# Kernel tuning notes

Hardware: AMD Instinct MI355X
Metric: run time of the kernel (lower is better)

The kernel has to match this reference:

```python
import jax, jax.numpy as jnp
import numpy as np

EMB = 1024

def setup_inputs() -> dict:
    key = jax.random.key(0)
    ks = jax.random.split(key, 7)
    s = 1.0 / np.sqrt(EMB)
    x = jax.random.normal(ks[0], (4, 2048, EMB), dtype=jnp.float32)
    Wk = jax.random.normal(ks[1], (EMB, EMB), dtype=jnp.float32) * s
    bk = jnp.zeros((EMB,), dtype=jnp.float32)
    Wq = jax.random.normal(ks[2], (EMB, EMB), dtype=jnp.float32) * s
    bq = jnp.zeros((EMB,), dtype=jnp.float32)
    Wv = jax.random.normal(ks[3], (EMB, EMB), dtype=jnp.float32) * s
    bv = jnp.zeros((EMB,), dtype=jnp.float32)
    return {"x": x, "Wk": Wk, "bk": bk, "Wq": Wq, "bq": bq, "Wv": Wv, "bv": bv}

def reference(x, Wk, bk, Wq, bq, Wv, bv):
    # Linear layers: x @ W.T + b (torch nn.Linear convention)
    k = jnp.einsum('bse,fe->bsf', x, Wk) + bk
    q = jnp.einsum('bse,fe->bsf', x, Wq) + bq
    v = jnp.einsum('bse,fe->bsf', x, Wv) + bv
    E = x.shape[-1]
    # NOTE: original computes k @ q^T (not q @ k^T) — reproduce faithfully.
    sim = jnp.einsum('bsd,btd->bst', k, q) / jnp.sqrt(jnp.float32(E))
    S = x.shape[1]
    causal = jnp.tril(jnp.ones((S, S), dtype=bool))  # [S,S]
    sim = jnp.where(causal, sim, -jnp.inf)
    attn = jax.nn.softmax(sim, axis=-1)
    return jnp.einsum('bst,btd->bsd', attn, v)
```

## Files before the change

### kernel.cpp

```cpp
#include <hip/hip_runtime.h>
#include <cstdint>


typedef __attribute__((ext_vector_type(8))) _Float16 f16x8;
typedef __attribute__((ext_vector_type(4))) float f32x4;

__device__ __forceinline__ unsigned short f2h(float x) {
  return __builtin_bit_cast(unsigned short, (_Float16)x);
}

__device__ __forceinline__ void lds_dma16(const void* g, void* l) {
  auto gp = reinterpret_cast<const __attribute__((address_space(1))) void*>(
      reinterpret_cast<uintptr_t>(g));
  auto lp = reinterpret_cast<__attribute__((address_space(3))) void*>(
      reinterpret_cast<uintptr_t>(l));
  __builtin_amdgcn_global_load_lds(gp, lp, 16, 0, 0);
}

__device__ __forceinline__ void gemm128(const unsigned short* __restrict__ Ag,
                                        const unsigned short* __restrict__ Bg,
                                        int lda, int ldb, int nk,
                                        unsigned short* As, unsigned short* Bs,
                                        f32x4 acc[4][4]) {
  const int tid = threadIdx.x;
  const int lane = tid & 63, wave = tid >> 6;
  const int wm = wave >> 1, wn = wave & 1;
  const int sr = lane >> 2;
  const int scb = (((lane & 3) ^ ((lane >> 3) & 3)) * 8);
  const int rr = lane & 15, qq = lane >> 4;
  const int slot = ((qq ^ ((rr >> 1) & 3)) * 8);

#pragma unroll
  for (int i = 0; i < 4; ++i)
#pragma unroll
    for (int j = 0; j < 4; ++j) {
      f32x4 z = {0.f, 0.f, 0.f, 0.f};
      acc[i][j] = z;
    }

  for (int k0 = 0; k0 < nk; k0 += 32) {
#pragma unroll
    for (int c = 0; c < 2; ++c) {
      int chunk = wave * 2 + c;
      int row = chunk * 16 + sr;
      lds_dma16(Ag + (size_t)row * lda + k0 + scb, As + chunk * 512);
      lds_dma16(Bg + (size_t)row * ldb + k0 + scb, Bs + chunk * 512);
    }
    __syncthreads();

    f16x8 af[4], bf[4];
    const unsigned short* Ar = As + (wm * 64 + rr) * 32 + slot;
    const unsigned short* Br = Bs + (wn * 64 + rr) * 32 + slot;
#pragma unroll
    for (int i = 0; i < 4; ++i) af[i] = *(const f16x8*)(Ar + i * 512);
#pragma unroll
    for (int j = 0; j < 4; ++j) bf[j] = *(const f16x8*)(Br + j * 512);
#pragma unroll
    for (int i = 0; i < 4; ++i)
#pragma unroll
      for (int j = 0; j < 4; ++j)
        acc[i][j] = __builtin_amdgcn_mfma_f32_16x16x32_f16(af[i], bf[j],
                                                           acc[i][j], 0, 0, 0);
    __syncthreads();
  }
}

__global__ void cvt_kernel(const float* __restrict__ x,
                           const float* __restrict__ w0,
                           const float* __restrict__ w1,
                           const float* __restrict__ w2,
                           unsigned short* __restrict__ dst) {
  int i = blockIdx.x * 256 + threadIdx.x;
  const float* s;
  size_t si;
  if (i < 2097152) {
    s = x; si = i;
  } else {
    int j = i - 2097152;
    int z = j >> 18;
    s = (z == 0) ? w0 : ((z == 1) ? w1 : w2);
    si = j & 262143;
  }
  float4 f = ((const float4*)s)[si];
  ushort4 u;
  u.x = f2h(f.x); u.y = f2h(f.y); u.z = f2h(f.z); u.w = f2h(f.w);
  ((ushort4*)dst)[i] = u;
}

__global__ __launch_bounds__(256) void qkv_gemm_kernel(
    const unsigned short* __restrict__ xh, const unsigned short* __restrict__ wh,
    const float* __restrict__ bk, const float* __restrict__ bq,
    const float* __restrict__ bv, unsigned short* __restrict__ kh,
    unsigned short* __restrict__ qh, unsigned short* __restrict__ vh) {
  __shared__ unsigned short As[128 * 32], Bs[128 * 32];
  const int tn = blockIdx.x & 7, z = blockIdx.x >> 3;
  const unsigned short* W = wh + (size_t)z * 1048576;
  const float* bias = (z == 0) ? bk : ((z == 1) ? bq : bv);
  unsigned short* dst = (z == 0) ? kh : ((z == 1) ? qh : vh);
  const int tm = blockIdx.y;

  f32x4 acc[4][4];
  gemm128(xh + (size_t)tm * 128 * 1024, W + (size_t)tn * 128 * 1024,
          1024, 1024, 1024, As, Bs, acc);

  const int lane = threadIdx.x & 63, wave = threadIdx.x >> 6;
  const int wm = wave >> 1, wn = wave & 1, rr = lane & 15, qq = lane >> 4;
  float bj[4];
#pragma unroll
  for (int j = 0; j < 4; ++j)
    bj[j] = bias[tn * 128 + wn * 64 + j * 16 + rr];
#pragma unroll
  for (int i = 0; i < 4; ++i)
#pragma unroll
    for (int reg = 0; reg < 4; ++reg) {
      int gm = tm * 128 + wm * 64 + i * 16 + qq * 4 + reg;
#pragma unroll
      for (int j = 0; j < 4; ++j) {
        int gc = tn * 128 + wn * 64 + j * 16 + rr;
        dst[(size_t)gm * 1024 + gc] = f2h(acc[i][j][reg] + bj[j]);
      }
    }
}

__global__ void transpose_v_kernel(const unsigned short* __restrict__ v,
                                   unsigned short* __restrict__ vT) {
  __shared__ unsigned short tile[32][33];
  const int b = blockIdx.z;
  const unsigned short* vp = v + (size_t)b * 2048 * 1024;
  unsigned short* vtp = vT + (size_t)b * 1024 * 2048;
  const int t0 = blockIdx.x * 32, d0 = blockIdx.y * 32;
  const int x = threadIdx.x, y = threadIdx.y;
#pragma unroll
  for (int i = 0; i < 32; i += 8)
    tile[y + i][x] = vp[(size_t)(t0 + y + i) * 1024 + d0 + x];
  __syncthreads();
#pragma unroll
  for (int i = 0; i < 32; i += 8)
    vtp[(size_t)(d0 + y + i) * 2048 + t0 + x] = tile[x][y + i];
}

__global__ __launch_bounds__(256) void scores_kernel(
    const unsigned short* __restrict__ kh, const unsigned short* __restrict__ qh,
    unsigned short* __restrict__ P, float* __restrict__ rsum) {
  const int tt = blockIdx.x, ts = blockIdx.y, b = blockIdx.z;
  if (tt > ts) return;
  __shared__ unsigned short As[128 * 32], Bs[128 * 32];

  f32x4 acc[4][4];
  gemm128(kh + ((size_t)(b * 2048 + ts * 128)) * 1024,
          qh + ((size_t)(b * 2048 + tt * 128)) * 1024,
          1024, 1024, 1024, As, Bs, acc);

  const int lane = threadIdx.x & 63, wave = threadIdx.x >> 6;
  const int wm = wave >> 1, wn = wave & 1, rr = lane & 15, qq = lane >> 4;
  unsigned short* Pb = P + (size_t)b * 2048 * 2048;
  float* rs = rsum + b * 2048;
#pragma unroll
  for (int i = 0; i < 4; ++i)
#pragma unroll
    for (int reg = 0; reg < 4; ++reg) {
      int srow = ts * 128 + wm * 64 + i * 16 + qq * 4 + reg;
      float p = 0.f;
#pragma unroll
      for (int j = 0; j < 4; ++j) {
        int tcol = tt * 128 + wn * 64 + j * 16 + rr;
        float e = (tcol <= srow) ? __expf(acc[i][j][reg] * 0.03125f - 4.0f)
                                 : 0.0f;
        Pb[(size_t)srow * 2048 + tcol] = f2h(e);
        p += e;
      }
#pragma unroll
      for (int off = 1; off < 16; off <<= 1) p += __shfl_xor(p, off);
      if (rr == 0) atomicAdd(rs + srow, p);
    }
}

__global__ __launch_bounds__(256) void pv_gemm_kernel(
    const unsigned short* __restrict__ P, const unsigned short* __restrict__ vT,
    const float* __restrict__ rsum, float* __restrict__ out) {
  const int td = blockIdx.x, ts = 15 - blockIdx.y, b = blockIdx.z;
  __shared__ unsigned short As[128 * 32], Bs[128 * 32];

  f32x4 acc[4][4];
  gemm128(P + ((size_t)(b * 2048 + ts * 128)) * 2048,
          vT + ((size_t)(b * 1024 + td * 128)) * 2048,
          2048, 2048, (ts + 1) * 128, As, Bs, acc);

  const int lane = threadIdx.x & 63, wave = threadIdx.x >> 6;
  const int wm = wave >> 1, wn = wave & 1, rr = lane & 15, qq = lane >> 4;
#pragma unroll
  for (int i = 0; i < 4; ++i)
#pragma unroll
    for (int reg = 0; reg < 4; ++reg) {
      int srow = ts * 128 + wm * 64 + i * 16 + qq * 4 + reg;
      float rv = __builtin_amdgcn_rcpf(rsum[b * 2048 + srow]);
#pragma unroll
      for (int j = 0; j < 4; ++j) {
        int dcol = td * 128 + wn * 64 + j * 16 + rr;
        out[((size_t)(b * 2048 + srow)) * 1024 + dcol] = acc[i][j][reg] * rv;
      }
    }
}

extern "C" void kernel_launch(void* const* d_in, const int* in_sizes, int n_in,
                              void* d_out, int out_size, void* d_ws,
                              size_t ws_size, hipStream_t stream) {
  const float* x  = (const float*)d_in[0];
  const float* Wk = (const float*)d_in[1];
  const float* bk = (const float*)d_in[2];
  const float* Wq = (const float*)d_in[3];
  const float* bq = (const float*)d_in[4];
  const float* Wv = (const float*)d_in[5];
  const float* bv = (const float*)d_in[6];
  float* out = (float*)d_out;

  char* ws = (char*)d_ws;
  const size_t MB = 1ull << 20;
  unsigned short* xh = (unsigned short*)(ws + 0);
  unsigned short* wh = (unsigned short*)(ws + 16 * MB);
  unsigned short* vh = (unsigned short*)(ws + 22 * MB);
  unsigned short* P  = (unsigned short*)(ws + 0);
  unsigned short* kh = (unsigned short*)(ws + 38 * MB);
  unsigned short* qh = (unsigned short*)(ws + 54 * MB);
  unsigned short* vT = (unsigned short*)(ws + 70 * MB);
  float* rsum = (float*)(ws + 86 * MB);

  hipMemsetAsync(rsum, 0, 8192 * sizeof(float), stream);
  cvt_kernel<<<11264, 256, 0, stream>>>(x, Wk, Wq, Wv, xh);
  qkv_gemm_kernel<<<dim3(24, 64), 256, 0, stream>>>(xh, wh, bk, bq, bv,
                                                    kh, qh, vh);
  transpose_v_kernel<<<dim3(64, 32, 4), dim3(32, 8), 0, stream>>>(vh, vT);
  scores_kernel<<<dim3(16, 16, 4), 256, 0, stream>>>(kh, qh, P, rsum);
  pv_gemm_kernel<<<dim3(8, 16, 4), 256, 0, stream>>>(P, vT, rsum, out);
}
```

Baseline: 277.2 us.

## Double GEMM K-step to 64, fold rsum clear, vectorize transpose, compact causal grid

The shared GEMM loop now stages 64-wide K slices per barrier pair, with a new XOR swizzle, which halves the number of syncthreads and gives each wave more MFMA work per load. The rsum memset is folded into the conversion kernel as extra threads. The V transpose uses 64x64 tiles with ushort4 global accesses. The scores launch maps a linear index onto lower-triangle tiles only, so no blocks exit early. Doubling the LDS tile per block may reduce occupancy.

```diff
diff --git a/kernel.cpp b/kernel.cpp
--- a/kernel.cpp
+++ b/kernel.cpp
@@ -25,10 +25,11 @@
   const int tid = threadIdx.x;
   const int lane = tid & 63, wave = tid >> 6;
   const int wm = wave >> 1, wn = wave & 1;
-  const int sr = lane >> 2;
-  const int scb = (((lane & 3) ^ ((lane >> 3) & 3)) * 8);
+  const int sr = lane >> 3;
+  const int scb = ((lane & 7) ^ sr) * 8;
   const int rr = lane & 15, qq = lane >> 4;
-  const int slot = ((qq ^ ((rr >> 1) & 3)) * 8);
+  const int slot0 = ((qq) ^ (rr & 7)) * 8;
+  const int slot1 = ((4 + qq) ^ (rr & 7)) * 8;
 
 #pragma unroll
   for (int i = 0; i < 4; ++i)
@@ -38,29 +39,44 @@
       acc[i][j] = z;
     }
 
-  for (int k0 = 0; k0 < nk; k0 += 32) {
-#pragma unroll
-    for (int c = 0; c < 2; ++c) {
-      int chunk = wave * 2 + c;
-      int row = chunk * 16 + sr;
+  for (int k0 = 0; k0 < nk; k0 += 64) {
+#pragma unroll
+    for (int c = 0; c < 4; ++c) {
+      int chunk = wave * 4 + c;
+      int row = chunk * 8 + sr;
       lds_dma16(Ag + (size_t)row * lda + k0 + scb, As + chunk * 512);
       lds_dma16(Bg + (size_t)row * ldb + k0 + scb, Bs + chunk * 512);
     }
     __syncthreads();
 
-    f16x8 af[4], bf[4];
-    const unsigned short* Ar = As + (wm * 64 + rr) * 32 + slot;
-    const unsigned short* Br = Bs + (wn * 64 + rr) * 32 + slot;
-#pragma unroll
-    for (int i = 0; i < 4; ++i) af[i] = *(const f16x8*)(Ar + i * 512);
-#pragma unroll
-    for (int j = 0; j < 4; ++j) bf[j] = *(const f16x8*)(Br + j * 512);
-#pragma unroll
-    for (int i = 0; i < 4; ++i)
-#pragma unroll
-      for (int j = 0; j < 4; ++j)
-        acc[i][j] = __builtin_amdgcn_mfma_f32_16x16x32_f16(af[i], bf[j],
-                                                           acc[i][j], 0, 0, 0);
+    const unsigned short* Ar = As + (wm * 64 + rr) * 64;
+    const unsigned short* Br = Bs + (wn * 64 + rr) * 64;
+    {
+      f16x8 af[4], bf[4];
+#pragma unroll
+      for (int i = 0; i < 4; ++i) af[i] = *(const f16x8*)(Ar + i * 1024 + slot0);
+#pragma unroll
+      for (int j = 0; j < 4; ++j) bf[j] = *(const f16x8*)(Br + j * 1024 + slot0);
+#pragma unroll
+      for (int i = 0; i < 4; ++i)
+#pragma unroll
+        for (int j = 0; j < 4; ++j)
+          acc[i][j] = __builtin_amdgcn_mfma_f32_16x16x32_f16(af[i], bf[j],
+                                                             acc[i][j], 0, 0, 0);
+    }
+    {
+      f16x8 af[4], bf[4];
+#pragma unroll
+      for (int i = 0; i < 4; ++i) af[i] = *(const f16x8*)(Ar + i * 1024 + slot1);
+#pragma unroll
+      for (int j = 0; j < 4; ++j) bf[j] = *(const f16x8*)(Br + j * 1024 + slot1);
+#pragma unroll
+      for (int i = 0; i < 4; ++i)
+#pragma unroll
+        for (int j = 0; j < 4; ++j)
+          acc[i][j] = __builtin_amdgcn_mfma_f32_16x16x32_f16(af[i], bf[j],
+                                                             acc[i][j], 0, 0, 0);
+    }
     __syncthreads();
   }
 }
@@ -69,8 +85,15 @@
                            const float* __restrict__ w0,
                            const float* __restrict__ w1,
                            const float* __restrict__ w2,
-                           unsigned short* __restrict__ dst) {
+                           unsigned short* __restrict__ dst,
+                           float* __restrict__ rsum) {
   int i = blockIdx.x * 256 + threadIdx.x;
+  if (i >= 2883584) {
+    int z2 = i - 2883584;
+    float4 z = {0.f, 0.f, 0.f, 0.f};
+    ((float4*)rsum)[z2] = z;
+    return;
+  }
   const float* s;
   size_t si;
   if (i < 2097152) {
@@ -92,7 +115,7 @@
     const float* __restrict__ bk, const float* __restrict__ bq,
     const float* __restrict__ bv, unsigned short* __restrict__ kh,
     unsigned short* __restrict__ qh, unsigned short* __restrict__ vh) {
-  __shared__ unsigned short As[128 * 32], Bs[128 * 32];
+  __shared__ unsigned short As[128 * 64], Bs[128 * 64];
   const int tn = blockIdx.x & 7, z = blockIdx.x >> 3;
   const unsigned short* W = wh + (size_t)z * 1048576;
   const float* bias = (z == 0) ? bk : ((z == 1) ? bq : bv);
@@ -122,29 +145,42 @@
     }
 }
 
-__global__ void transpose_v_kernel(const unsigned short* __restrict__ v,
-                                   unsigned short* __restrict__ vT) {
-  __shared__ unsigned short tile[32][33];
+__global__ __launch_bounds__(256) void transpose_v_kernel(
+    const unsigned short* __restrict__ v, unsigned short* __restrict__ vT) {
+  __shared__ unsigned short tile[64][65];
   const int b = blockIdx.z;
   const unsigned short* vp = v + (size_t)b * 2048 * 1024;
   unsigned short* vtp = vT + (size_t)b * 1024 * 2048;
-  const int t0 = blockIdx.x * 32, d0 = blockIdx.y * 32;
-  const int x = threadIdx.x, y = threadIdx.y;
-#pragma unroll
-  for (int i = 0; i < 32; i += 8)
-    tile[y + i][x] = vp[(size_t)(t0 + y + i) * 1024 + d0 + x];
+  const int t0 = blockIdx.x * 64, d0 = blockIdx.y * 64;
+  const int lr = threadIdx.x >> 4, lc = (threadIdx.x & 15) * 4;
+#pragma unroll
+  for (int p = 0; p < 4; ++p) {
+    int tr = p * 16 + lr;
+    ushort4 u = *(const ushort4*)(vp + (size_t)(t0 + tr) * 1024 + d0 + lc);
+    tile[tr][lc] = u.x; tile[tr][lc + 1] = u.y;
+    tile[tr][lc + 2] = u.z; tile[tr][lc + 3] = u.w;
+  }
   __syncthreads();
 #pragma unroll
-  for (int i = 0; i < 32; i += 8)
-    vtp[(size_t)(d0 + y + i) * 2048 + t0 + x] = tile[x][y + i];
+  for (int p = 0; p < 4; ++p) {
+    int dr = p * 16 + lr;
+    ushort4 u;
+    u.x = tile[lc][dr]; u.y = tile[lc + 1][dr];
+    u.z = tile[lc + 2][dr]; u.w = tile[lc + 3][dr];
+    *(ushort4*)(vtp + (size_t)(d0 + dr) * 2048 + t0 + lc) = u;
+  }
 }
 
 __global__ __launch_bounds__(256) void scores_kernel(
     const unsigned short* __restrict__ kh, const unsigned short* __restrict__ qh,
     unsigned short* __restrict__ P, float* __restrict__ rsum) {
-  const int tt = blockIdx.x, ts = blockIdx.y, b = blockIdx.z;
-  if (tt > ts) return;
-  __shared__ unsigned short As[128 * 32], Bs[128 * 32];
+  const int b = blockIdx.y;
+  int idx = blockIdx.x;
+  int ts = (int)((sqrtf(8.0f * idx + 1.0f) - 1.0f) * 0.5f);
+  while ((ts + 1) * (ts + 2) / 2 <= idx) ++ts;
+  while (ts * (ts + 1) / 2 > idx) --ts;
+  const int tt = idx - ts * (ts + 1) / 2;
+  __shared__ unsigned short As[128 * 64], Bs[128 * 64];
 
   f32x4 acc[4][4];
   gemm128(kh + ((size_t)(b * 2048 + ts * 128)) * 1024,
@@ -179,7 +215,7 @@
     const unsigned short* __restrict__ P, const unsigned short* __restrict__ vT,
     const float* __restrict__ rsum, float* __restrict__ out) {
   const int td = blockIdx.x, ts = 15 - blockIdx.y, b = blockIdx.z;
-  __shared__ unsigned short As[128 * 32], Bs[128 * 32];
+  __shared__ unsigned short As[128 * 64], Bs[128 * 64];
 
   f32x4 acc[4][4];
   gemm128(P + ((size_t)(b * 2048 + ts * 128)) * 2048,
@@ -225,11 +261,10 @@
   unsigned short* vT = (unsigned short*)(ws + 70 * MB);
   float* rsum = (float*)(ws + 86 * MB);
 
-  hipMemsetAsync(rsum, 0, 8192 * sizeof(float), stream);
-  cvt_kernel<<<11264, 256, 0, stream>>>(x, Wk, Wq, Wv, xh);
+  cvt_kernel<<<11272, 256, 0, stream>>>(x, Wk, Wq, Wv, xh, rsum);
   qkv_gemm_kernel<<<dim3(24, 64), 256, 0, stream>>>(xh, wh, bk, bq, bv,
                                                     kh, qh, vh);
-  transpose_v_kernel<<<dim3(64, 32, 4), dim3(32, 8), 0, stream>>>(vh, vT);
-  scores_kernel<<<dim3(16, 16, 4), 256, 0, stream>>>(kh, qh, P, rsum);
+  transpose_v_kernel<<<dim3(32, 16, 4), 256, 0, stream>>>(vh, vT);
+  scores_kernel<<<dim3(136, 4), 256, 0, stream>>>(kh, qh, P, rsum);
   pv_gemm_kernel<<<dim3(8, 16, 4), 256, 0, stream>>>(P, vT, rsum, out);
 }
```

Result: faster. 266.9 us (-3.7%).
